# Performance work log

Measured on AMD Instinct MI355X. Metric: run time of the kernel, lower is better.

## Reference

```python
import jax, jax.numpy as jnp
import numpy as np

N, F_IN, D, R, E = 50000, 128, 96, 2, 800000


def setup_inputs() -> dict:
    key = jax.random.key(0)
    ks = jax.random.split(key, 8)
    sc = lambda k, shape: jax.random.normal(k, shape, jnp.float32) * 0.05
    return {
        "x": jax.random.normal(ks[0], (N, F_IN), jnp.float32),
        "edge_index": jax.random.randint(ks[1], (2, E), 0, N),
        "edge_attr": jax.random.uniform(ks[2], (E, R), dtype=jnp.float32),
        # nn.Linear(F_IN, D)
        "Wf": sc(ks[3], (D, F_IN)),
        "bf": jnp.zeros((D,), jnp.float32),
        # RGCNConv: per-relation weights, root weight, bias
        "W": sc(ks[4], (R, D, D)),
        "root": sc(ks[5], (D, D)),
        "bias": jnp.zeros((D,), jnp.float32),
    }


def _rgcn_conv(h, src, dst, etype, W, root, bias):
    # PyG RGCNConv (no bases/blocks, aggr='mean'):
    #   out = x @ root + bias + sum_r mean_{edges of type r}(x[src]) @ W[r]
    msg = h[src]  # [E, D] gather
    out = h @ root + bias
    for r in range(R):
        w = (etype == r).astype(h.dtype)[:, None]  # [E, 1] relation mask
        s = jax.ops.segment_sum(msg * w, dst, num_segments=N)   # [N, D] scatter-add
        cnt = jax.ops.segment_sum(w, dst, num_segments=N)       # [N, 1]
        agg = s / jnp.maximum(cnt, 1.0)                          # mean, safe for deg 0
        out = out + agg @ W[r]
    return out


def reference(x, edge_index, edge_attr, Wf, bf, W, root, bias):
    src, dst = edge_index[0], edge_index[1]
    etype = jnp.argmax(edge_attr, axis=1)  # [E]
    h = jax.nn.relu(x @ Wf.T + bf)
    for _ in range(3):
        h = jax.nn.relu(_rgcn_conv(h, src, dst, etype, W, root, bias))
    return h
```

## Files before the change

kernel.cpp:

```cpp
#include <hip/hip_runtime.h>

#define DN 96
#define FIN 128

typedef unsigned int uint_t;
typedef unsigned short ushort_t;

typedef __attribute__((ext_vector_type(8))) short short8v;
typedef __attribute__((ext_vector_type(4))) float f32x4;

#define MFMA16 __builtin_amdgcn_mfma_f32_16x16x32_bf16

struct __align__(4) U3 { uint_t x, y, z; };

__device__ __forceinline__ ushort_t f2bf(float f) {
    uint_t u = __float_as_uint(f);
    uint_t r = (u + 0x7FFFu + ((u >> 16) & 1u)) >> 16;
    return (ushort_t)r;
}
__device__ __forceinline__ float bf2f(ushort_t h) { return __uint_as_float(((uint_t)h) << 16); }
__device__ __forceinline__ float bf_lo(uint_t u) { return __uint_as_float(u << 16); }
__device__ __forceinline__ float bf_hi(uint_t u) { return __uint_as_float(u & 0xFFFF0000u); }


__global__ void hist_kernel(const int* __restrict__ ei, const float* __restrict__ ea,
                            int* __restrict__ cnt, uint2* __restrict__ kd, int E, int N) {
    int e = blockIdx.x * 256 + threadIdx.x;
    if (e >= E) return;
    int src = ei[e];
    int dst = ei[E + e];
    int r = (ea[2 * e + 1] > ea[2 * e]) ? 1 : 0;
    kd[e] = make_uint2((uint_t)dst | ((uint_t)r << 16), (uint_t)src);
    atomicAdd(&cnt[r * N + dst], 1);
}

__global__ void offsets_kernel(const int* __restrict__ cnt, int* __restrict__ total,
                               int* __restrict__ rowstart, int* __restrict__ fillptr,
                               int nbins) {
    __shared__ int sd[256];
    __shared__ int sbase;
    int t = threadIdx.x;
    int b = blockIdx.x * 256 + t;
    int v = (b < nbins) ? cnt[b] : 0;
    sd[t] = v;
    __syncthreads();
    for (int off = 1; off < 256; off <<= 1) {
        int add = (t >= off) ? sd[t - off] : 0;
        __syncthreads();
        sd[t] += add;
        __syncthreads();
    }
    if (t == 255) sbase = atomicAdd(total, sd[255]);
    __syncthreads();
    if (b < nbins) {
        int s = sbase + sd[t] - v;
        rowstart[b] = s;
        fillptr[b] = s;
    }
}


__global__ __launch_bounds__(256) void fill_part(const uint2* __restrict__ kd,
                            int* __restrict__ fillptr, int* __restrict__ srcs,
                            int E, int N, int PS) {
    int p = blockIdx.x & 7;
    int c = blockIdx.x >> 3;
    int base = c * 2048 + threadIdx.x;
#pragma unroll
    for (int i = 0; i < 8; i++) {
        int e = base + i * 256;
        if (e < E) {
            uint2 v = kd[e];
            int dst = v.x & 0xFFFF;
            if (dst / PS == p) {
                int r = (v.x >> 16) & 1;
                int pos = atomicAdd(&fillptr[r * N + dst], 1);
                srcs[pos] = (int)v.y;
            }
        }
    }
}


__global__ void pack_all(const float* __restrict__ root, const float* __restrict__ W,
                         const float* __restrict__ Wf,
                         ushort_t* __restrict__ Bph, ushort_t* __restrict__ Bpl,
                         ushort_t* __restrict__ Wfh, ushort_t* __restrict__ Wfl) {
    int l = threadIdx.x;
    int bid = blockIdx.x;
    if (bid < 54) {
        int fid = bid;
        int ct = fid / 3, ks = fid % 3;
        int mat = ct / 6, cw = ct % 6;
        const float* M = (mat == 0) ? root : (W + (size_t)(mat - 1) * DN * DN);
        int k0 = 32 * ks + (l >> 4) * 8;
        int col = 16 * cw + (l & 15);
#pragma unroll
        for (int j = 0; j < 8; j++) {
            float v = M[(size_t)(k0 + j) * DN + col];
            ushort_t h = f2bf(v);
            size_t idx = ((size_t)fid * 64 + l) * 8 + j;
            Bph[idx] = h;
            Bpl[idx] = f2bf(v - bf2f(h));
        }
    } else {
        int fid = bid - 54;
        int ct = fid >> 2, ks = fid & 3;
        int k0 = 32 * ks + (l >> 4) * 8;
        int col = 16 * ct + (l & 15);
#pragma unroll
        for (int j = 0; j < 8; j++) {
            float v = Wf[(size_t)col * FIN + k0 + j];
            ushort_t h = f2bf(v);
            size_t idx = ((size_t)fid * 64 + l) * 8 + j;
            Wfh[idx] = h;
            Wfl[idx] = f2bf(v - bf2f(h));
        }
    }
}


__device__ __forceinline__ void cvt8(float4 x, float4 y, short8v& hi, short8v& lo) {
    union { short8v v; ushort_t u[8]; } H, L;
    float f[8] = {x.x, x.y, x.z, x.w, y.x, y.y, y.z, y.w};
#pragma unroll
    for (int j = 0; j < 8; j++) {
        ushort_t h = f2bf(f[j]);
        H.u[j] = h;
        L.u[j] = f2bf(f[j] - bf2f(h));
    }
    hi = H.v; lo = L.v;
}


template <int MODE>
__global__ __launch_bounds__(256) void layer_kernel(
    const float* __restrict__ xin,
    const float* __restrict__ hrootIn,
    const uint_t* __restrict__ g0In, const uint_t* __restrict__ g1In,
    const int* __restrict__ rowstart, const int* __restrict__ cnt,
    const int* __restrict__ srcs,
    const ushort_t* __restrict__ WfH, const ushort_t* __restrict__ WfL,
    const ushort_t* __restrict__ Bph, const ushort_t* __restrict__ Bpl,
    const float* __restrict__ bfv, const float* __restrict__ bias,
    float* __restrict__ hrootOut, ushort_t* __restrict__ g0Out, ushort_t* __restrict__ g1Out,
    float* __restrict__ dout, int N)
{
    constexpr int NW = (MODE == 0) ? 4 : 1;
    __shared__ float sout[NW][16][100];
    int t = threadIdx.x;
    int l = t & 63;
    int w = t >> 6;

    if constexpr (MODE == 0) {
        int slab = blockIdx.x * 64 + w * 16;
        int row = slab + (l & 15);
        if (row >= N) row = N - 1;
        const float* xrow = xin + (size_t)row * FIN + ((l >> 4) * 8);
        short8v ah[4], al[4];
#pragma unroll
        for (int ks = 0; ks < 4; ks++) {
            float4 xa = *(const float4*)(xrow + 32 * ks);
            float4 xb = *(const float4*)(xrow + 32 * ks + 4);
            cvt8(xa, xb, ah[ks], al[ks]);
        }
#pragma unroll
        for (int ct = 0; ct < 6; ct++) {
            f32x4 hh = {0.f,0.f,0.f,0.f}, hl_ = {0.f,0.f,0.f,0.f}, lh = {0.f,0.f,0.f,0.f};
#pragma unroll
            for (int ks = 0; ks < 4; ks++) {
                size_t base = ((size_t)(ct * 4 + ks) * 64 + l) * 8;
                short8v bh = *(const short8v*)(WfH + base);
                short8v bl = *(const short8v*)(WfL + base);
                hh  = MFMA16(ah[ks], bh, hh, 0, 0, 0);
                hl_ = MFMA16(ah[ks], bl, hl_, 0, 0, 0);
                lh  = MFMA16(al[ks], bh, lh, 0, 0, 0);
            }
            f32x4 acc = hh + hl_ + lh;
            int col = ct * 16 + (l & 15);
            float bv = bfv[col];
            int lr0 = (l >> 4) * 4;
#pragma unroll
            for (int r = 0; r < 4; r++) {
                float v = acc[r] + bv;
                sout[w][lr0 + r][col] = v > 0.f ? v : 0.f;
            }
        }
    } else {
        int grp = t >> 4;
        int j = t & 15;
        int n = blockIdx.x * 16 + grp;
        bool valid = n < N;
        int nc = valid ? n : N - 1;
        float a0=0.f,a1=0.f,a2=0.f,a3=0.f,a4=0.f,a5=0.f;
#pragma unroll
        for (int r = 0; r < 2; r++) {
            int c    = valid ? cnt[r * N + nc] : 0;
            int base = valid ? rowstart[r * N + nc] : 0;
            const uint_t* g = r ? g1In : g0In;
            const int* sp = srcs + base;
            float s0=0.f,s1=0.f,s2=0.f,s3=0.f,s4=0.f,s5=0.f;
            int e = 0;
            for (; e + 4 <= c; e += 4) {
                int i0 = sp[e], i1 = sp[e+1], i2 = sp[e+2], i3 = sp[e+3];
                U3 v0 = *(const U3*)(g + (size_t)i0 * 48 + 3 * j);
                U3 v1 = *(const U3*)(g + (size_t)i1 * 48 + 3 * j);
                U3 v2 = *(const U3*)(g + (size_t)i2 * 48 + 3 * j);
                U3 v3 = *(const U3*)(g + (size_t)i3 * 48 + 3 * j);
                s0 += (bf_lo(v0.x) + bf_lo(v1.x)) + (bf_lo(v2.x) + bf_lo(v3.x));
                s1 += (bf_hi(v0.x) + bf_hi(v1.x)) + (bf_hi(v2.x) + bf_hi(v3.x));
                s2 += (bf_lo(v0.y) + bf_lo(v1.y)) + (bf_lo(v2.y) + bf_lo(v3.y));
                s3 += (bf_hi(v0.y) + bf_hi(v1.y)) + (bf_hi(v2.y) + bf_hi(v3.y));
                s4 += (bf_lo(v0.z) + bf_lo(v1.z)) + (bf_lo(v2.z) + bf_lo(v3.z));
                s5 += (bf_hi(v0.z) + bf_hi(v1.z)) + (bf_hi(v2.z) + bf_hi(v3.z));
            }
            for (; e < c; e++) {
                U3 v = *(const U3*)(g + (size_t)sp[e] * 48 + 3 * j);
                s0 += bf_lo(v.x); s1 += bf_hi(v.x);
                s2 += bf_lo(v.y); s3 += bf_hi(v.y);
                s4 += bf_lo(v.z); s5 += bf_hi(v.z);
            }
            float inv = (c > 0) ? 1.f / (float)c : 0.f;
            a0 += s0 * inv; a1 += s1 * inv; a2 += s2 * inv;
            a3 += s3 * inv; a4 += s4 * inv; a5 += s5 * inv;
        }
        const float* hr = hrootIn + (size_t)nc * DN + 6 * j;
        float2 p0 = *(const float2*)hr;
        float2 p1 = *(const float2*)(hr + 2);
        float2 p2 = *(const float2*)(hr + 4);
        float o0 = fmaxf(p0.x + a0, 0.f);
        float o1 = fmaxf(p0.y + a1, 0.f);
        float o2 = fmaxf(p1.x + a2, 0.f);
        float o3 = fmaxf(p1.y + a3, 0.f);
        float o4 = fmaxf(p2.x + a4, 0.f);
        float o5 = fmaxf(p2.y + a5, 0.f);
        if constexpr (MODE == 1) {
            float* dr = &sout[0][grp][6 * j];
            dr[0]=o0; dr[1]=o1; dr[2]=o2; dr[3]=o3; dr[4]=o4; dr[5]=o5;
        } else {
            if (valid) {
                float* dr = dout + (size_t)n * DN + 6 * j;
                *(float2*)(dr)     = make_float2(o0, o1);
                *(float2*)(dr + 2) = make_float2(o2, o3);
                *(float2*)(dr + 4) = make_float2(o4, o5);
            }
        }
    }

    if constexpr (MODE == 2) return;
    __syncthreads();

    {
        const float* srow;
        int mbase;
        if constexpr (MODE == 0) {
            srow = &sout[w][l & 15][0];
            mbase = blockIdx.x * 64 + w * 16 + ((l >> 4) << 2);
        } else {
            srow = &sout[0][l & 15][0];
            mbase = blockIdx.x * 16 + ((l >> 4) << 2);
        }
        int k0 = (l >> 4) * 8;
        short8v ah[3], al[3];
#pragma unroll
        for (int ks = 0; ks < 3; ks++) {
            float4 xa = *(const float4*)(srow + k0 + 32 * ks);
            float4 xb = *(const float4*)(srow + k0 + 32 * ks + 4);
            cvt8(xa, xb, ah[ks], al[ks]);
        }
        int ctS, ctC;
        if constexpr (MODE == 0) { ctS = 0; ctC = 18; }
        else { ctS = (w < 2) ? 5 * w : 10 + 4 * (w - 2); ctC = (w < 2) ? 5 : 4; }
        for (int ci = 0; ci < ctC; ci++) {
            int ct = ctS + ci;
            f32x4 hh = {0.f,0.f,0.f,0.f}, hl_ = {0.f,0.f,0.f,0.f}, lh = {0.f,0.f,0.f,0.f};
#pragma unroll
            for (int ks = 0; ks < 3; ks++) {
                size_t base = ((size_t)(ct * 3 + ks) * 64 + l) * 8;
                short8v bh = *(const short8v*)(Bph + base);
                short8v bl = *(const short8v*)(Bpl + base);
                hh  = MFMA16(ah[ks], bh, hh, 0, 0, 0);
                hl_ = MFMA16(ah[ks], bl, hl_, 0, 0, 0);
                lh  = MFMA16(al[ks], bh, lh, 0, 0, 0);
            }
            f32x4 acc = hh + hl_ + lh;
            int mat = ct / 6;
            int col = (ct % 6) * 16 + (l & 15);
            if (mat == 0) {
                float bv = bias[col];
#pragma unroll
                for (int r = 0; r < 4; r++) {
                    int m = mbase + r;
                    if (m < N) hrootOut[(size_t)m * DN + col] = acc[r] + bv;
                }
            } else {
                ushort_t* g = (mat == 1) ? g0Out : g1Out;
#pragma unroll
                for (int r = 0; r < 4; r++) {
                    int m = mbase + r;
                    if (m < N) g[(size_t)m * DN + col] = f2bf(acc[r]);
                }
            }
        }
    }
}

extern "C" void kernel_launch(void* const* d_in, const int* in_sizes, int n_in,
                              void* d_out, int out_size, void* d_ws, size_t ws_size,
                              hipStream_t stream) {
    const float* x    = (const float*)d_in[0];
    const int*   ei   = (const int*)d_in[1];
    const float* ea   = (const float*)d_in[2];
    const float* Wf   = (const float*)d_in[3];
    const float* bf   = (const float*)d_in[4];
    const float* W    = (const float*)d_in[5];
    const float* root = (const float*)d_in[6];
    const float* bias = (const float*)d_in[7];
    float* out = (float*)d_out;

    int N = in_sizes[0] / FIN;
    int E = in_sizes[1] / 2;
    int nbins = 2 * N;
    int PS = (N + 7) / 8;

    int* cnt      = (int*)d_ws;
    int* total    = cnt + nbins;
    int* rowstart = cnt + nbins + 4;
    int* fillptr  = rowstart + nbins;
    int* srcs     = fillptr + nbins;
    uint2* kd     = (uint2*)(srcs + E);
    ushort_t* Bph = (ushort_t*)(kd + E);
    ushort_t* Bpl = Bph + 54 * 512;
    ushort_t* Wfh = Bpl + 54 * 512;
    ushort_t* Wfl = Wfh + 24 * 512;
    float* hrootA = (float*)(Wfl + 24 * 512);
    ushort_t* g0A = (ushort_t*)(hrootA + (size_t)N * DN);
    ushort_t* g1A = g0A + (size_t)N * DN;
    float* hrootB = (float*)(g1A + (size_t)N * DN);
    ushort_t* g0B = (ushort_t*)(hrootB + (size_t)N * DN);
    ushort_t* g1B = g0B + (size_t)N * DN;

    hipMemsetAsync(cnt, 0, (size_t)(nbins + 1) * sizeof(int), stream);

    hist_kernel<<<(E + 255) / 256, 256, 0, stream>>>(ei, ea, cnt, kd, E, N);
    offsets_kernel<<<(nbins + 255) / 256, 256, 0, stream>>>(cnt, total, rowstart, fillptr, nbins);
    int nchunk = (E + 2047) / 2048;
    fill_part<<<nchunk * 8, 256, 0, stream>>>(kd, fillptr, srcs, E, N, PS);
    pack_all<<<78, 64, 0, stream>>>(root, W, Wf, Bph, Bpl, Wfh, Wfl);

    int blk64 = (N + 63) / 64;
    int blk16 = (N + 15) / 16;

    layer_kernel<0><<<blk64, 256, 0, stream>>>(
        x, nullptr, nullptr, nullptr, rowstart, cnt, srcs,
        Wfh, Wfl, Bph, Bpl, bf, bias, hrootA, g0A, g1A, nullptr, N);
    layer_kernel<1><<<blk16, 256, 0, stream>>>(
        nullptr, hrootA, (const uint_t*)g0A, (const uint_t*)g1A, rowstart, cnt, srcs,
        nullptr, nullptr, Bph, Bpl, nullptr, bias, hrootB, g0B, g1B, nullptr, N);
    layer_kernel<1><<<blk16, 256, 0, stream>>>(
        nullptr, hrootB, (const uint_t*)g0B, (const uint_t*)g1B, rowstart, cnt, srcs,
        nullptr, nullptr, Bph, Bpl, nullptr, bias, hrootA, g0A, g1A, nullptr, N);
    layer_kernel<2><<<blk16, 256, 0, stream>>>(
        nullptr, hrootA, (const uint_t*)g0A, (const uint_t*)g1A, rowstart, cnt, srcs,
        nullptr, nullptr, nullptr, nullptr, nullptr, nullptr, nullptr, nullptr, nullptr, out, N);
}
```

Baseline: 294.3 us.

## Split gather across two half-waves per node and interleave relation loads

The aggregation kernel now uses 512 threads per block, with 32 lanes per destination node. Each half of those lanes takes alternate edges, and the halves are combined with a shuffle. The loops for the two relations are interleaved so eight independent row gathers are in flight per iteration, which adds memory-level parallelism to a latency-bound gather. The first-layer linear GEMM moves into its own kernel. The per-block MFMA work is redistributed across 8 waves, which costs some register pressure and more partial-edge handling.

```diff
diff --git a/kernel.cpp b/kernel.cpp
--- a/kernel.cpp
+++ b/kernel.cpp
@@ -21,6 +21,15 @@
 __device__ __forceinline__ float bf2f(ushort_t h) { return __uint_as_float(((uint_t)h) << 16); }
 __device__ __forceinline__ float bf_lo(uint_t u) { return __uint_as_float(u << 16); }
 __device__ __forceinline__ float bf_hi(uint_t u) { return __uint_as_float(u & 0xFFFF0000u); }
+
+__device__ __forceinline__ U3 ldrow(const uint_t* __restrict__ g, int idx, int j) {
+    return *(const U3*)(g + (size_t)idx * 48 + 3 * j);
+}
+__device__ __forceinline__ void acc6(float* s, U3 v) {
+    s[0] += bf_lo(v.x); s[1] += bf_hi(v.x);
+    s[2] += bf_lo(v.y); s[3] += bf_hi(v.y);
+    s[4] += bf_lo(v.z); s[5] += bf_hi(v.z);
+}
 
 
 __global__ void hist_kernel(const int* __restrict__ ei, const float* __restrict__ ea,
@@ -133,133 +142,199 @@
 }
 
 
-template <int MODE>
-__global__ __launch_bounds__(256) void layer_kernel(
+__global__ __launch_bounds__(256) void lin_gemm(
     const float* __restrict__ xin,
+    const ushort_t* __restrict__ WfH, const ushort_t* __restrict__ WfL,
+    const ushort_t* __restrict__ Bph, const ushort_t* __restrict__ Bpl,
+    const float* __restrict__ bfv, const float* __restrict__ bias,
+    float* __restrict__ hrootOut, ushort_t* __restrict__ g0Out, ushort_t* __restrict__ g1Out,
+    int N)
+{
+    __shared__ float sout[4][16][100];
+    int t = threadIdx.x;
+    int l = t & 63;
+    int w = t >> 6;
+
+    int slab = blockIdx.x * 64 + w * 16;
+    int row = slab + (l & 15);
+    if (row >= N) row = N - 1;
+    const float* xrow = xin + (size_t)row * FIN + ((l >> 4) * 8);
+    short8v ah4[4], al4[4];
+#pragma unroll
+    for (int ks = 0; ks < 4; ks++) {
+        float4 xa = *(const float4*)(xrow + 32 * ks);
+        float4 xb = *(const float4*)(xrow + 32 * ks + 4);
+        cvt8(xa, xb, ah4[ks], al4[ks]);
+    }
+#pragma unroll
+    for (int ct = 0; ct < 6; ct++) {
+        f32x4 hh = {0.f,0.f,0.f,0.f}, hl_ = {0.f,0.f,0.f,0.f}, lh = {0.f,0.f,0.f,0.f};
+#pragma unroll
+        for (int ks = 0; ks < 4; ks++) {
+            size_t base = ((size_t)(ct * 4 + ks) * 64 + l) * 8;
+            short8v bh = *(const short8v*)(WfH + base);
+            short8v bl = *(const short8v*)(WfL + base);
+            hh  = MFMA16(ah4[ks], bh, hh, 0, 0, 0);
+            hl_ = MFMA16(ah4[ks], bl, hl_, 0, 0, 0);
+            lh  = MFMA16(al4[ks], bh, lh, 0, 0, 0);
+        }
+        f32x4 acc = hh + hl_ + lh;
+        int col = ct * 16 + (l & 15);
+        float bv = bfv[col];
+        int lr0 = (l >> 4) * 4;
+#pragma unroll
+        for (int r = 0; r < 4; r++) {
+            float v = acc[r] + bv;
+            sout[w][lr0 + r][col] = v > 0.f ? v : 0.f;
+        }
+    }
+    __syncthreads();
+
+    const float* srow = &sout[w][l & 15][0];
+    int mbase = blockIdx.x * 64 + w * 16 + ((l >> 4) << 2);
+    int k0 = (l >> 4) * 8;
+    short8v ah[3], al[3];
+#pragma unroll
+    for (int ks = 0; ks < 3; ks++) {
+        float4 xa = *(const float4*)(srow + k0 + 32 * ks);
+        float4 xb = *(const float4*)(srow + k0 + 32 * ks + 4);
+        cvt8(xa, xb, ah[ks], al[ks]);
+    }
+    for (int ct = 0; ct < 18; ct++) {
+        f32x4 hh = {0.f,0.f,0.f,0.f}, hl_ = {0.f,0.f,0.f,0.f}, lh = {0.f,0.f,0.f,0.f};
+#pragma unroll
+        for (int ks = 0; ks < 3; ks++) {
+            size_t base = ((size_t)(ct * 3 + ks) * 64 + l) * 8;
+            short8v bh = *(const short8v*)(Bph + base);
+            short8v bl = *(const short8v*)(Bpl + base);
+            hh  = MFMA16(ah[ks], bh, hh, 0, 0, 0);
+            hl_ = MFMA16(ah[ks], bl, hl_, 0, 0, 0);
+            lh  = MFMA16(al[ks], bh, lh, 0, 0, 0);
+        }
+        f32x4 acc = hh + hl_ + lh;
+        int mat = ct / 6;
+        int col = (ct % 6) * 16 + (l & 15);
+        if (mat == 0) {
+            float bv = bias[col];
+#pragma unroll
+            for (int r = 0; r < 4; r++) {
+                int m = mbase + r;
+                if (m < N) hrootOut[(size_t)m * DN + col] = acc[r] + bv;
+            }
+        } else {
+            ushort_t* g = (mat == 1) ? g0Out : g1Out;
+#pragma unroll
+            for (int r = 0; r < 4; r++) {
+                int m = mbase + r;
+                if (m < N) g[(size_t)m * DN + col] = f2bf(acc[r]);
+            }
+        }
+    }
+}
+
+
+template <int GEMM>
+__global__ __launch_bounds__(512, 4) void layer_kernel(
     const float* __restrict__ hrootIn,
     const uint_t* __restrict__ g0In, const uint_t* __restrict__ g1In,
     const int* __restrict__ rowstart, const int* __restrict__ cnt,
     const int* __restrict__ srcs,
-    const ushort_t* __restrict__ WfH, const ushort_t* __restrict__ WfL,
     const ushort_t* __restrict__ Bph, const ushort_t* __restrict__ Bpl,
-    const float* __restrict__ bfv, const float* __restrict__ bias,
+    const float* __restrict__ bias,
     float* __restrict__ hrootOut, ushort_t* __restrict__ g0Out, ushort_t* __restrict__ g1Out,
     float* __restrict__ dout, int N)
 {
-    constexpr int NW = (MODE == 0) ? 4 : 1;
-    __shared__ float sout[NW][16][100];
+    __shared__ float sout[16][100];
     int t = threadIdx.x;
-    int l = t & 63;
-    int w = t >> 6;
-
-    if constexpr (MODE == 0) {
-        int slab = blockIdx.x * 64 + w * 16;
-        int row = slab + (l & 15);
-        if (row >= N) row = N - 1;
-        const float* xrow = xin + (size_t)row * FIN + ((l >> 4) * 8);
-        short8v ah[4], al[4];
-#pragma unroll
-        for (int ks = 0; ks < 4; ks++) {
-            float4 xa = *(const float4*)(xrow + 32 * ks);
-            float4 xb = *(const float4*)(xrow + 32 * ks + 4);
-            cvt8(xa, xb, ah[ks], al[ks]);
-        }
-#pragma unroll
-        for (int ct = 0; ct < 6; ct++) {
-            f32x4 hh = {0.f,0.f,0.f,0.f}, hl_ = {0.f,0.f,0.f,0.f}, lh = {0.f,0.f,0.f,0.f};
-#pragma unroll
-            for (int ks = 0; ks < 4; ks++) {
-                size_t base = ((size_t)(ct * 4 + ks) * 64 + l) * 8;
-                short8v bh = *(const short8v*)(WfH + base);
-                short8v bl = *(const short8v*)(WfL + base);
-                hh  = MFMA16(ah[ks], bh, hh, 0, 0, 0);
-                hl_ = MFMA16(ah[ks], bl, hl_, 0, 0, 0);
-                lh  = MFMA16(al[ks], bh, lh, 0, 0, 0);
-            }
-            f32x4 acc = hh + hl_ + lh;
-            int col = ct * 16 + (l & 15);
-            float bv = bfv[col];
-            int lr0 = (l >> 4) * 4;
-#pragma unroll
-            for (int r = 0; r < 4; r++) {
-                float v = acc[r] + bv;
-                sout[w][lr0 + r][col] = v > 0.f ? v : 0.f;
-            }
-        }
-    } else {
-        int grp = t >> 4;
-        int j = t & 15;
+
+    {
+        int grp = t >> 5;
+        int l32 = t & 31;
+        int j = l32 & 15;
+        int sub = l32 >> 4;
         int n = blockIdx.x * 16 + grp;
         bool valid = n < N;
         int nc = valid ? n : N - 1;
-        float a0=0.f,a1=0.f,a2=0.f,a3=0.f,a4=0.f,a5=0.f;
-#pragma unroll
-        for (int r = 0; r < 2; r++) {
-            int c    = valid ? cnt[r * N + nc] : 0;
-            int base = valid ? rowstart[r * N + nc] : 0;
-            const uint_t* g = r ? g1In : g0In;
-            const int* sp = srcs + base;
-            float s0=0.f,s1=0.f,s2=0.f,s3=0.f,s4=0.f,s5=0.f;
-            int e = 0;
-            for (; e + 4 <= c; e += 4) {
-                int i0 = sp[e], i1 = sp[e+1], i2 = sp[e+2], i3 = sp[e+3];
-                U3 v0 = *(const U3*)(g + (size_t)i0 * 48 + 3 * j);
-                U3 v1 = *(const U3*)(g + (size_t)i1 * 48 + 3 * j);
-                U3 v2 = *(const U3*)(g + (size_t)i2 * 48 + 3 * j);
-                U3 v3 = *(const U3*)(g + (size_t)i3 * 48 + 3 * j);
-                s0 += (bf_lo(v0.x) + bf_lo(v1.x)) + (bf_lo(v2.x) + bf_lo(v3.x));
-                s1 += (bf_hi(v0.x) + bf_hi(v1.x)) + (bf_hi(v2.x) + bf_hi(v3.x));
-                s2 += (bf_lo(v0.y) + bf_lo(v1.y)) + (bf_lo(v2.y) + bf_lo(v3.y));
-                s3 += (bf_hi(v0.y) + bf_hi(v1.y)) + (bf_hi(v2.y) + bf_hi(v3.y));
-                s4 += (bf_lo(v0.z) + bf_lo(v1.z)) + (bf_lo(v2.z) + bf_lo(v3.z));
-                s5 += (bf_hi(v0.z) + bf_hi(v1.z)) + (bf_hi(v2.z) + bf_hi(v3.z));
-            }
-            for (; e < c; e++) {
-                U3 v = *(const U3*)(g + (size_t)sp[e] * 48 + 3 * j);
-                s0 += bf_lo(v.x); s1 += bf_hi(v.x);
-                s2 += bf_lo(v.y); s3 += bf_hi(v.y);
-                s4 += bf_lo(v.z); s5 += bf_hi(v.z);
-            }
-            float inv = (c > 0) ? 1.f / (float)c : 0.f;
-            a0 += s0 * inv; a1 += s1 * inv; a2 += s2 * inv;
-            a3 += s3 * inv; a4 += s4 * inv; a5 += s5 * inv;
-        }
-        const float* hr = hrootIn + (size_t)nc * DN + 6 * j;
-        float2 p0 = *(const float2*)hr;
-        float2 p1 = *(const float2*)(hr + 2);
-        float2 p2 = *(const float2*)(hr + 4);
-        float o0 = fmaxf(p0.x + a0, 0.f);
-        float o1 = fmaxf(p0.y + a1, 0.f);
-        float o2 = fmaxf(p1.x + a2, 0.f);
-        float o3 = fmaxf(p1.y + a3, 0.f);
-        float o4 = fmaxf(p2.x + a4, 0.f);
-        float o5 = fmaxf(p2.y + a5, 0.f);
-        if constexpr (MODE == 1) {
-            float* dr = &sout[0][grp][6 * j];
-            dr[0]=o0; dr[1]=o1; dr[2]=o2; dr[3]=o3; dr[4]=o4; dr[5]=o5;
-        } else {
-            if (valid) {
-                float* dr = dout + (size_t)n * DN + 6 * j;
-                *(float2*)(dr)     = make_float2(o0, o1);
-                *(float2*)(dr + 2) = make_float2(o2, o3);
-                *(float2*)(dr + 4) = make_float2(o4, o5);
-            }
-        }
-    }
-
-    if constexpr (MODE == 2) return;
+        int c0 = valid ? cnt[nc] : 0;
+        int b0 = valid ? rowstart[nc] : 0;
+        int c1 = valid ? cnt[N + nc] : 0;
+        int b1 = valid ? rowstart[N + nc] : 0;
+
+        float2 ph0, ph1, ph2;
+        if (sub == 0) {
+            const float* hr = hrootIn + (size_t)nc * DN + 6 * j;
+            ph0 = *(const float2*)hr;
+            ph1 = *(const float2*)(hr + 2);
+            ph2 = *(const float2*)(hr + 4);
+        }
+
+        float sA[6] = {0.f,0.f,0.f,0.f,0.f,0.f};
+        float sB[6] = {0.f,0.f,0.f,0.f,0.f,0.f};
+        const int* q0 = srcs + b0 + sub;
+        const int* q1 = srcs + b1 + sub;
+        int m0 = (c0 + 1 - sub) >> 1;
+        int m1 = (c1 + 1 - sub) >> 1;
+        int i0 = 0, i1 = 0;
+        while (i0 + 4 <= m0 && i1 + 4 <= m1) {
+            U3 a0 = ldrow(g0In, q0[0], j), a1 = ldrow(g0In, q0[2], j);
+            U3 a2 = ldrow(g0In, q0[4], j), a3 = ldrow(g0In, q0[6], j);
+            U3 b0v = ldrow(g1In, q1[0], j), b1v = ldrow(g1In, q1[2], j);
+            U3 b2v = ldrow(g1In, q1[4], j), b3v = ldrow(g1In, q1[6], j);
+            acc6(sA, a0); acc6(sA, a1); acc6(sA, a2); acc6(sA, a3);
+            acc6(sB, b0v); acc6(sB, b1v); acc6(sB, b2v); acc6(sB, b3v);
+            q0 += 8; q1 += 8; i0 += 4; i1 += 4;
+        }
+        while (i0 + 4 <= m0) {
+            U3 a0 = ldrow(g0In, q0[0], j), a1 = ldrow(g0In, q0[2], j);
+            U3 a2 = ldrow(g0In, q0[4], j), a3 = ldrow(g0In, q0[6], j);
+            acc6(sA, a0); acc6(sA, a1); acc6(sA, a2); acc6(sA, a3);
+            q0 += 8; i0 += 4;
+        }
+        while (i1 + 4 <= m1) {
+            U3 b0v = ldrow(g1In, q1[0], j), b1v = ldrow(g1In, q1[2], j);
+            U3 b2v = ldrow(g1In, q1[4], j), b3v = ldrow(g1In, q1[6], j);
+            acc6(sB, b0v); acc6(sB, b1v); acc6(sB, b2v); acc6(sB, b3v);
+            q1 += 8; i1 += 4;
+        }
+        for (; i0 < m0; i0++) { U3 v = ldrow(g0In, q0[0], j); acc6(sA, v); q0 += 2; }
+        for (; i1 < m1; i1++) { U3 v = ldrow(g1In, q1[0], j); acc6(sB, v); q1 += 2; }
+
+#pragma unroll
+        for (int k = 0; k < 6; k++) {
+            sA[k] += __shfl_xor(sA[k], 16);
+            sB[k] += __shfl_xor(sB[k], 16);
+        }
+        if (sub == 0) {
+            float inv0 = (c0 > 0) ? 1.f / (float)c0 : 0.f;
+            float inv1 = (c1 > 0) ? 1.f / (float)c1 : 0.f;
+            float o0 = fmaxf(ph0.x + sA[0] * inv0 + sB[0] * inv1, 0.f);
+            float o1 = fmaxf(ph0.y + sA[1] * inv0 + sB[1] * inv1, 0.f);
+            float o2 = fmaxf(ph1.x + sA[2] * inv0 + sB[2] * inv1, 0.f);
+            float o3 = fmaxf(ph1.y + sA[3] * inv0 + sB[3] * inv1, 0.f);
+            float o4 = fmaxf(ph2.x + sA[4] * inv0 + sB[4] * inv1, 0.f);
+            float o5 = fmaxf(ph2.y + sA[5] * inv0 + sB[5] * inv1, 0.f);
+            if constexpr (GEMM) {
+                float* dr = &sout[grp][6 * j];
+                dr[0]=o0; dr[1]=o1; dr[2]=o2; dr[3]=o3; dr[4]=o4; dr[5]=o5;
+            } else {
+                if (valid) {
+                    float* dr = dout + (size_t)n * DN + 6 * j;
+                    *(float2*)(dr)     = make_float2(o0, o1);
+                    *(float2*)(dr + 2) = make_float2(o2, o3);
+                    *(float2*)(dr + 4) = make_float2(o4, o5);
+                }
+            }
+        }
+    }
+
+    if constexpr (!GEMM) return;
     __syncthreads();
 
     {
-        const float* srow;
-        int mbase;
-        if constexpr (MODE == 0) {
-            srow = &sout[w][l & 15][0];
-            mbase = blockIdx.x * 64 + w * 16 + ((l >> 4) << 2);
-        } else {
-            srow = &sout[0][l & 15][0];
-            mbase = blockIdx.x * 16 + ((l >> 4) << 2);
-        }
+        int l = t & 63;
+        int w = t >> 6;
+        const float* srow = &sout[l & 15][0];
+        int mbase = blockIdx.x * 16 + ((l >> 4) << 2);
         int k0 = (l >> 4) * 8;
         short8v ah[3], al[3];
 #pragma unroll
@@ -268,9 +343,8 @@
             float4 xb = *(const float4*)(srow + k0 + 32 * ks + 4);
             cvt8(xa, xb, ah[ks], al[ks]);
         }
-        int ctS, ctC;
-        if constexpr (MODE == 0) { ctS = 0; ctC = 18; }
-        else { ctS = (w < 2) ? 5 * w : 10 + 4 * (w - 2); ctC = (w < 2) ? 5 : 4; }
+        int ctC = (w < 2) ? 3 : 2;
+        int ctS = (w < 2) ? 3 * w : 6 + 2 * (w - 2);
         for (int ci = 0; ci < ctC; ci++) {
             int ct = ctS + ci;
             f32x4 hh = {0.f,0.f,0.f,0.f}, hl_ = {0.f,0.f,0.f,0.f}, lh = {0.f,0.f,0.f,0.f};
@@ -351,16 +425,15 @@
     int blk64 = (N + 63) / 64;
     int blk16 = (N + 15) / 16;
 
-    layer_kernel<0><<<blk64, 256, 0, stream>>>(
-        x, nullptr, nullptr, nullptr, rowstart, cnt, srcs,
-        Wfh, Wfl, Bph, Bpl, bf, bias, hrootA, g0A, g1A, nullptr, N);
-    layer_kernel<1><<<blk16, 256, 0, stream>>>(
-        nullptr, hrootA, (const uint_t*)g0A, (const uint_t*)g1A, rowstart, cnt, srcs,
-        nullptr, nullptr, Bph, Bpl, nullptr, bias, hrootB, g0B, g1B, nullptr, N);
-    layer_kernel<1><<<blk16, 256, 0, stream>>>(
-        nullptr, hrootB, (const uint_t*)g0B, (const uint_t*)g1B, rowstart, cnt, srcs,
-        nullptr, nullptr, Bph, Bpl, nullptr, bias, hrootA, g0A, g1A, nullptr, N);
-    layer_kernel<2><<<blk16, 256, 0, stream>>>(
-        nullptr, hrootA, (const uint_t*)g0A, (const uint_t*)g1A, rowstart, cnt, srcs,
-        nullptr, nullptr, nullptr, nullptr, nullptr, nullptr, nullptr, nullptr, nullptr, out, N);
-}
+    lin_gemm<<<blk64, 256, 0, stream>>>(
+        x, Wfh, Wfl, Bph, Bpl, bf, bias, hrootA, g0A, g1A, N);
+    layer_kernel<1><<<blk16, 512, 0, stream>>>(
+        hrootA, (const uint_t*)g0A, (const uint_t*)g1A, rowstart, cnt, srcs,
+        Bph, Bpl, bias, hrootB, g0B, g1B, nullptr, N);
+    layer_kernel<1><<<blk16, 512, 0, stream>>>(
+        hrootB, (const uint_t*)g0B, (const uint_t*)g1B, rowstart, cnt, srcs,
+        Bph, Bpl, bias, hrootA, g0A, g1A, nullptr, N);
+    layer_kernel<0><<<blk16, 512, 0, stream>>>(
+        hrootA, (const uint_t*)g0A, (const uint_t*)g1A, rowstart, cnt, srcs,
+        nullptr, nullptr, nullptr, nullptr, nullptr, nullptr, out, N);
+}
```

Result: slower. 359.7 us (+22.2%).

## Sort nodes by degree so aggregation blocks get balanced edge counts

Applied to the files above, without the earlier changes.

Adds three small kernels that build a degree histogram, scan it, and scatter node ids into a permutation ordered by descending total in-degree. The aggregation and GEMM layer kernels then process nodes through this permutation and write outputs indirectly via a shared-memory index table. The intent is to cut intra-wavefront divergence in the per-node gather loops, since the 16 nodes handled together now have similar edge counts. The cost is three extra launches, atomics, and less locality in the hroot and output stores, which now go to scattered rows. The input linear layer moves into its own kernel, which is structural only.

```diff
diff --git a/kernel.cpp b/kernel.cpp
--- a/kernel.cpp
+++ b/kernel.cpp
@@ -82,6 +82,40 @@
 }
 
 
+__global__ void deg_hist(const int* __restrict__ cnt, int* __restrict__ dhist, int N) {
+    int n = blockIdx.x * 256 + threadIdx.x;
+    if (n >= N) return;
+    int d = cnt[n] + cnt[N + n];
+    if (d > 127) d = 127;
+    atomicAdd(&dhist[127 - d], 1);
+}
+
+__global__ void deg_scan(const int* __restrict__ dhist, int* __restrict__ dfill) {
+    __shared__ int s[128];
+    int t = threadIdx.x;
+    int v = dhist[t];
+    s[t] = v;
+    __syncthreads();
+    for (int off = 1; off < 128; off <<= 1) {
+        int a = (t >= off) ? s[t - off] : 0;
+        __syncthreads();
+        s[t] += a;
+        __syncthreads();
+    }
+    dfill[t] = s[t] - v;
+}
+
+__global__ void deg_scatter(const int* __restrict__ cnt, int* __restrict__ dfill,
+                            int* __restrict__ perm, int N) {
+    int n = blockIdx.x * 256 + threadIdx.x;
+    if (n >= N) return;
+    int d = cnt[n] + cnt[N + n];
+    if (d > 127) d = 127;
+    int pos = atomicAdd(&dfill[127 - d], 1);
+    perm[pos] = n;
+}
+
+
 __global__ void pack_all(const float* __restrict__ root, const float* __restrict__ W,
                          const float* __restrict__ Wf,
                          ushort_t* __restrict__ Bph, ushort_t* __restrict__ Bpl,
@@ -133,65 +167,121 @@
 }
 
 
-template <int MODE>
+__global__ __launch_bounds__(256) void lin_gemm(
+    const float* __restrict__ xin,
+    const ushort_t* __restrict__ WfH, const ushort_t* __restrict__ WfL,
+    const ushort_t* __restrict__ Bph, const ushort_t* __restrict__ Bpl,
+    const float* __restrict__ bfv, const float* __restrict__ bias,
+    float* __restrict__ hrootOut, ushort_t* __restrict__ g0Out, ushort_t* __restrict__ g1Out,
+    int N)
+{
+    __shared__ float sout[4][16][100];
+    int t = threadIdx.x;
+    int l = t & 63;
+    int w = t >> 6;
+
+    int slab = blockIdx.x * 64 + w * 16;
+    int row = slab + (l & 15);
+    if (row >= N) row = N - 1;
+    const float* xrow = xin + (size_t)row * FIN + ((l >> 4) * 8);
+    short8v ah4[4], al4[4];
+#pragma unroll
+    for (int ks = 0; ks < 4; ks++) {
+        float4 xa = *(const float4*)(xrow + 32 * ks);
+        float4 xb = *(const float4*)(xrow + 32 * ks + 4);
+        cvt8(xa, xb, ah4[ks], al4[ks]);
+    }
+#pragma unroll
+    for (int ct = 0; ct < 6; ct++) {
+        f32x4 hh = {0.f,0.f,0.f,0.f}, hl_ = {0.f,0.f,0.f,0.f}, lh = {0.f,0.f,0.f,0.f};
+#pragma unroll
+        for (int ks = 0; ks < 4; ks++) {
+            size_t base = ((size_t)(ct * 4 + ks) * 64 + l) * 8;
+            short8v bh = *(const short8v*)(WfH + base);
+            short8v bl = *(const short8v*)(WfL + base);
+            hh  = MFMA16(ah4[ks], bh, hh, 0, 0, 0);
+            hl_ = MFMA16(ah4[ks], bl, hl_, 0, 0, 0);
+            lh  = MFMA16(al4[ks], bh, lh, 0, 0, 0);
+        }
+        f32x4 acc = hh + hl_ + lh;
+        int col = ct * 16 + (l & 15);
+        float bv = bfv[col];
+        int lr0 = (l >> 4) * 4;
+#pragma unroll
+        for (int r = 0; r < 4; r++) {
+            float v = acc[r] + bv;
+            sout[w][lr0 + r][col] = v > 0.f ? v : 0.f;
+        }
+    }
+    __syncthreads();
+
+    const float* srow = &sout[w][l & 15][0];
+    int mbase = blockIdx.x * 64 + w * 16 + ((l >> 4) << 2);
+    int k0 = (l >> 4) * 8;
+    short8v ah[3], al[3];
+#pragma unroll
+    for (int ks = 0; ks < 3; ks++) {
+        float4 xa = *(const float4*)(srow + k0 + 32 * ks);
+        float4 xb = *(const float4*)(srow + k0 + 32 * ks + 4);
+        cvt8(xa, xb, ah[ks], al[ks]);
+    }
+    for (int ct = 0; ct < 18; ct++) {
+        f32x4 hh = {0.f,0.f,0.f,0.f}, hl_ = {0.f,0.f,0.f,0.f}, lh = {0.f,0.f,0.f,0.f};
+#pragma unroll
+        for (int ks = 0; ks < 3; ks++) {
+            size_t base = ((size_t)(ct * 3 + ks) * 64 + l) * 8;
+            short8v bh = *(const short8v*)(Bph + base);
+            short8v bl = *(const short8v*)(Bpl + base);
+            hh  = MFMA16(ah[ks], bh, hh, 0, 0, 0);
+            hl_ = MFMA16(ah[ks], bl, hl_, 0, 0, 0);
+            lh  = MFMA16(al[ks], bh, lh, 0, 0, 0);
+        }
+        f32x4 acc = hh + hl_ + lh;
+        int mat = ct / 6;
+        int col = (ct % 6) * 16 + (l & 15);
+        if (mat == 0) {
+            float bv = bias[col];
+#pragma unroll
+            for (int r = 0; r < 4; r++) {
+                int m = mbase + r;
+                if (m < N) hrootOut[(size_t)m * DN + col] = acc[r] + bv;
+            }
+        } else {
+            ushort_t* g = (mat == 1) ? g0Out : g1Out;
+#pragma unroll
+            for (int r = 0; r < 4; r++) {
+                int m = mbase + r;
+                if (m < N) g[(size_t)m * DN + col] = f2bf(acc[r]);
+            }
+        }
+    }
+}
+
+
+template <int GEMM>
 __global__ __launch_bounds__(256) void layer_kernel(
-    const float* __restrict__ xin,
+    const int* __restrict__ perm,
     const float* __restrict__ hrootIn,
     const uint_t* __restrict__ g0In, const uint_t* __restrict__ g1In,
     const int* __restrict__ rowstart, const int* __restrict__ cnt,
     const int* __restrict__ srcs,
-    const ushort_t* __restrict__ WfH, const ushort_t* __restrict__ WfL,
     const ushort_t* __restrict__ Bph, const ushort_t* __restrict__ Bpl,
-    const float* __restrict__ bfv, const float* __restrict__ bias,
+    const float* __restrict__ bias,
     float* __restrict__ hrootOut, ushort_t* __restrict__ g0Out, ushort_t* __restrict__ g1Out,
     float* __restrict__ dout, int N)
 {
-    constexpr int NW = (MODE == 0) ? 4 : 1;
-    __shared__ float sout[NW][16][100];
+    __shared__ float sout[16][100];
+    __shared__ int sperm[16];
     int t = threadIdx.x;
-    int l = t & 63;
-    int w = t >> 6;
-
-    if constexpr (MODE == 0) {
-        int slab = blockIdx.x * 64 + w * 16;
-        int row = slab + (l & 15);
-        if (row >= N) row = N - 1;
-        const float* xrow = xin + (size_t)row * FIN + ((l >> 4) * 8);
-        short8v ah[4], al[4];
-#pragma unroll
-        for (int ks = 0; ks < 4; ks++) {
-            float4 xa = *(const float4*)(xrow + 32 * ks);
-            float4 xb = *(const float4*)(xrow + 32 * ks + 4);
-            cvt8(xa, xb, ah[ks], al[ks]);
-        }
-#pragma unroll
-        for (int ct = 0; ct < 6; ct++) {
-            f32x4 hh = {0.f,0.f,0.f,0.f}, hl_ = {0.f,0.f,0.f,0.f}, lh = {0.f,0.f,0.f,0.f};
-#pragma unroll
-            for (int ks = 0; ks < 4; ks++) {
-                size_t base = ((size_t)(ct * 4 + ks) * 64 + l) * 8;
-                short8v bh = *(const short8v*)(WfH + base);
-                short8v bl = *(const short8v*)(WfL + base);
-                hh  = MFMA16(ah[ks], bh, hh, 0, 0, 0);
-                hl_ = MFMA16(ah[ks], bl, hl_, 0, 0, 0);
-                lh  = MFMA16(al[ks], bh, lh, 0, 0, 0);
-            }
-            f32x4 acc = hh + hl_ + lh;
-            int col = ct * 16 + (l & 15);
-            float bv = bfv[col];
-            int lr0 = (l >> 4) * 4;
-#pragma unroll
-            for (int r = 0; r < 4; r++) {
-                float v = acc[r] + bv;
-                sout[w][lr0 + r][col] = v > 0.f ? v : 0.f;
-            }
-        }
-    } else {
+
+    {
         int grp = t >> 4;
         int j = t & 15;
-        int n = blockIdx.x * 16 + grp;
-        bool valid = n < N;
-        int nc = valid ? n : N - 1;
+        int idx = blockIdx.x * 16 + grp;
+        bool valid = idx < N;
+        int nc = valid ? perm[idx] : 0;
+        if (j == 0) sperm[grp] = valid ? nc : -1;
+
         float a0=0.f,a1=0.f,a2=0.f,a3=0.f,a4=0.f,a5=0.f;
 #pragma unroll
         for (int r = 0; r < 2; r++) {
@@ -234,12 +324,12 @@
         float o3 = fmaxf(p1.y + a3, 0.f);
         float o4 = fmaxf(p2.x + a4, 0.f);
         float o5 = fmaxf(p2.y + a5, 0.f);
-        if constexpr (MODE == 1) {
-            float* dr = &sout[0][grp][6 * j];
+        if constexpr (GEMM) {
+            float* dr = &sout[grp][6 * j];
             dr[0]=o0; dr[1]=o1; dr[2]=o2; dr[3]=o3; dr[4]=o4; dr[5]=o5;
         } else {
             if (valid) {
-                float* dr = dout + (size_t)n * DN + 6 * j;
+                float* dr = dout + (size_t)nc * DN + 6 * j;
                 *(float2*)(dr)     = make_float2(o0, o1);
                 *(float2*)(dr + 2) = make_float2(o2, o3);
                 *(float2*)(dr + 4) = make_float2(o4, o5);
@@ -247,19 +337,14 @@
         }
     }
 
-    if constexpr (MODE == 2) return;
+    if constexpr (!GEMM) return;
     __syncthreads();
 
     {
-        const float* srow;
-        int mbase;
-        if constexpr (MODE == 0) {
-            srow = &sout[w][l & 15][0];
-            mbase = blockIdx.x * 64 + w * 16 + ((l >> 4) << 2);
-        } else {
-            srow = &sout[0][l & 15][0];
-            mbase = blockIdx.x * 16 + ((l >> 4) << 2);
-        }
+        int l = t & 63;
+        int w = t >> 6;
+        const float* srow = &sout[l & 15][0];
+        int mrow0 = (l >> 4) << 2;
         int k0 = (l >> 4) * 8;
         short8v ah[3], al[3];
 #pragma unroll
@@ -269,8 +354,8 @@
             cvt8(xa, xb, ah[ks], al[ks]);
         }
         int ctS, ctC;
-        if constexpr (MODE == 0) { ctS = 0; ctC = 18; }
-        else { ctS = (w < 2) ? 5 * w : 10 + 4 * (w - 2); ctC = (w < 2) ? 5 : 4; }
+        ctS = (w < 2) ? 5 * w : 10 + 4 * (w - 2);
+        ctC = (w < 2) ? 5 : 4;
         for (int ci = 0; ci < ctC; ci++) {
             int ct = ctS + ci;
             f32x4 hh = {0.f,0.f,0.f,0.f}, hl_ = {0.f,0.f,0.f,0.f}, lh = {0.f,0.f,0.f,0.f};
@@ -290,15 +375,15 @@
                 float bv = bias[col];
 #pragma unroll
                 for (int r = 0; r < 4; r++) {
-                    int m = mbase + r;
-                    if (m < N) hrootOut[(size_t)m * DN + col] = acc[r] + bv;
+                    int m = sperm[mrow0 + r];
+                    if (m >= 0) hrootOut[(size_t)m * DN + col] = acc[r] + bv;
                 }
             } else {
                 ushort_t* g = (mat == 1) ? g0Out : g1Out;
 #pragma unroll
                 for (int r = 0; r < 4; r++) {
-                    int m = mbase + r;
-                    if (m < N) g[(size_t)m * DN + col] = f2bf(acc[r]);
+                    int m = sperm[mrow0 + r];
+                    if (m >= 0) g[(size_t)m * DN + col] = f2bf(acc[r]);
                 }
             }
         }
@@ -325,9 +410,12 @@
 
     int* cnt      = (int*)d_ws;
     int* total    = cnt + nbins;
-    int* rowstart = cnt + nbins + 4;
+    int* dhist    = cnt + nbins + 8;
+    int* dfill    = dhist + 128;
+    int* rowstart = dfill + 128;
     int* fillptr  = rowstart + nbins;
-    int* srcs     = fillptr + nbins;
+    int* perm     = fillptr + nbins;
+    int* srcs     = perm + N;
     uint2* kd     = (uint2*)(srcs + E);
     ushort_t* Bph = (ushort_t*)(kd + E);
     ushort_t* Bpl = Bph + 54 * 512;
@@ -340,27 +428,29 @@
     ushort_t* g0B = (ushort_t*)(hrootB + (size_t)N * DN);
     ushort_t* g1B = g0B + (size_t)N * DN;
 
-    hipMemsetAsync(cnt, 0, (size_t)(nbins + 1) * sizeof(int), stream);
+    hipMemsetAsync(cnt, 0, (size_t)(nbins + 8 + 128) * sizeof(int), stream);
 
     hist_kernel<<<(E + 255) / 256, 256, 0, stream>>>(ei, ea, cnt, kd, E, N);
     offsets_kernel<<<(nbins + 255) / 256, 256, 0, stream>>>(cnt, total, rowstart, fillptr, nbins);
     int nchunk = (E + 2047) / 2048;
     fill_part<<<nchunk * 8, 256, 0, stream>>>(kd, fillptr, srcs, E, N, PS);
+    deg_hist<<<(N + 255) / 256, 256, 0, stream>>>(cnt, dhist, N);
+    deg_scan<<<1, 128, 0, stream>>>(dhist, dfill);
+    deg_scatter<<<(N + 255) / 256, 256, 0, stream>>>(cnt, dfill, perm, N);
     pack_all<<<78, 64, 0, stream>>>(root, W, Wf, Bph, Bpl, Wfh, Wfl);
 
     int blk64 = (N + 63) / 64;
     int blk16 = (N + 15) / 16;
 
-    layer_kernel<0><<<blk64, 256, 0, stream>>>(
-        x, nullptr, nullptr, nullptr, rowstart, cnt, srcs,
-        Wfh, Wfl, Bph, Bpl, bf, bias, hrootA, g0A, g1A, nullptr, N);
+    lin_gemm<<<blk64, 256, 0, stream>>>(
+        x, Wfh, Wfl, Bph, Bpl, bf, bias, hrootA, g0A, g1A, N);
     layer_kernel<1><<<blk16, 256, 0, stream>>>(
-        nullptr, hrootA, (const uint_t*)g0A, (const uint_t*)g1A, rowstart, cnt, srcs,
-        nullptr, nullptr, Bph, Bpl, nullptr, bias, hrootB, g0B, g1B, nullptr, N);
+        perm, hrootA, (const uint_t*)g0A, (const uint_t*)g1A, rowstart, cnt, srcs,
+        Bph, Bpl, bias, hrootB, g0B, g1B, nullptr, N);
     layer_kernel<1><<<blk16, 256, 0, stream>>>(
-        nullptr, hrootB, (const uint_t*)g0B, (const uint_t*)g1B, rowstart, cnt, srcs,
-        nullptr, nullptr, Bph, Bpl, nullptr, bias, hrootA, g0A, g1A, nullptr, N);
-    layer_kernel<2><<<blk16, 256, 0, stream>>>(
-        nullptr, hrootA, (const uint_t*)g0A, (const uint_t*)g1A, rowstart, cnt, srcs,
-        nullptr, nullptr, nullptr, nullptr, nullptr, nullptr, nullptr, nullptr, nullptr, out, N);
-}
+        perm, hrootB, (const uint_t*)g0B, (const uint_t*)g1B, rowstart, cnt, srcs,
+        Bph, Bpl, bias, hrootA, g0A, g1A, nullptr, N);
+    layer_kernel<0><<<blk16, 256, 0, stream>>>(
+        perm, hrootA, (const uint_t*)g0A, (const uint_t*)g1A, rowstart, cnt, srcs,
+        nullptr, nullptr, nullptr, nullptr, nullptr, nullptr, out, N);
+}
```

Result: slower. 596.3 us (+102.6%).
